# Kernel tuning notes

Hardware: AMD Instinct MI355X
Metric: run time of the kernel (lower is better)

Reference implementation:

```python
import jax, jax.numpy as jnp
import numpy as np

CPJ = 8
HID = 256
PARENTS = [-1,0,0,0,1,2,3,4,5,6,7,8,9,9,9,12,13,14,16,17,18,19]
SPARSE_IDX = list(range(54))

def _extend(nodes, cpj, parents=None):
    nodes = list(nodes)
    if parents is not None:
        while nodes[-1] != 0:
            nodes.append(parents[nodes[-1]])
    return [j * cpj + k for j in nodes for k in range(cpj)]

DQ_IN = _extend([0,3,6,9,12,13,14,15,16,17,18,19,20,21], CPJ, PARENTS)  # 21 nodes -> 168 ch
OUT1 = _extend([9], CPJ)          # 8 ch
OUT2 = _extend([6, 9, 12], CPJ)   # 24 ch
OUT3 = _extend([0, 3, 6], CPJ)    # 24 ch
IN_DIM = len(DQ_IN) + len(SPARSE_IDX)  # 222


def _mlp_params(key, out_dim):
    k = jax.random.split(key, 6)
    s = lambda fan_in: 1.0 / np.sqrt(fan_in)
    return (
        jax.random.uniform(k[0], (IN_DIM, HID), jnp.float32, -s(IN_DIM), s(IN_DIM)),
        jax.random.uniform(k[1], (HID,), jnp.float32, -s(IN_DIM), s(IN_DIM)),
        jax.random.uniform(k[2], (HID, HID), jnp.float32, -s(HID), s(HID)),
        jax.random.uniform(k[3], (HID,), jnp.float32, -s(HID), s(HID)),
        jax.random.uniform(k[4], (HID, out_dim), jnp.float32, -s(HID), s(HID)),
        jax.random.uniform(k[5], (out_dim,), jnp.float32, -s(HID), s(HID)),
    )


def setup_inputs() -> dict:
    key = jax.random.key(0)
    ks = jax.random.split(key, 5)
    B, T = 1024, 128
    inp = {
        'sparse_input': jax.random.normal(ks[0], (B, T, 54), jnp.float32),
        'decoder_output': jax.random.normal(ks[1], (B, T, 22 * CPJ), jnp.float32),
    }
    for i, (k, od) in enumerate(zip(ks[2:5], (len(OUT1), len(OUT2), len(OUT3))), start=1):
        p = _mlp_params(k, od)
        for j, name in enumerate(('w0', 'b0', 'w1', 'b1', 'w2', 'b2')):
            inp[f'{name}_{i}'] = p[j]
    return inp


def _mlp(x, w0, b0, w1, b1, w2, b2):
    h = jax.nn.leaky_relu(x @ w0 + b0, 0.01)
    h = jax.nn.leaky_relu(h @ w1 + b1, 0.01)
    return h @ w2 + b2


def reference(sparse_input, decoder_output,
              w0_1, b0_1, w1_1, b1_1, w2_1, b2_1,
              w0_2, b0_2, w1_2, b1_2, w2_2, b2_2,
              w0_3, b0_3, w1_3, b1_3, w2_3, b2_3):
    sp = sparse_input[:, :, jnp.array(SPARSE_IDX)]
    d = decoder_output
    # pass 1
    x = jnp.concatenate((d[:, :, jnp.array(DQ_IN)], sp), axis=2)
    res1 = _mlp(x, w0_1, b0_1, w1_1, b1_1, w2_1, b2_1)
    d = d.at[:, :, jnp.array(OUT1)].set(res1)
    # pass 2
    x = jnp.concatenate((d[:, :, jnp.array(DQ_IN)], sp), axis=2)
    res2 = _mlp(x, w0_2, b0_2, w1_2, b1_2, w2_2, b2_2)
    d = d.at[:, :, jnp.array(OUT2)].set(res2)
    # pass 3
    x = jnp.concatenate((d[:, :, jnp.array(DQ_IN)], sp), axis=2)
    res3 = _mlp(x, w0_3, b0_3, w1_3, b1_3, w2_3, b2_3)
    return res3
```

## Files before the change

### kernel.cpp

```cpp
#include <hip/hip_runtime.h>

typedef __bf16 bf16x8 __attribute__((ext_vector_type(8)));
typedef __bf16 bf16x4 __attribute__((ext_vector_type(4)));
typedef float  f32x16 __attribute__((ext_vector_type(16)));

#define DDEC  176
#define DSP   54
#define HID   256
#define RPW   32
#define WPB   4
#define BM    (RPW * WPB)
#define CSZ   8192
#define PSZ   16384
#define W1_OFF 65536
#define W2_OFF 131072
#define MLP_WS 139264

struct Biases { const float* b1[3]; const float* b2[3]; };

__global__ __launch_bounds__(256) void prep_weights(
    const float* __restrict__ w0a, const float* __restrict__ w1a, const float* __restrict__ w2a,
    const float* __restrict__ w0b, const float* __restrict__ w1b, const float* __restrict__ w2b,
    const float* __restrict__ w0c, const float* __restrict__ w1c, const float* __restrict__ w2c,
    const float* __restrict__ b0a, const float* __restrict__ b0b, const float* __restrict__ b0c,
    __bf16* __restrict__ ws)
{
  int idx = blockIdx.x * 256 + threadIdx.x;
  if (idx >= 3 * MLP_WS) return;
  int m = idx / MLP_WS;
  int r = idx - m * MLP_WS;
  const float* w0 = (m == 0) ? w0a : (m == 1) ? w0b : w0c;
  const float* w1 = (m == 0) ? w1a : (m == 1) ? w1b : w1c;
  const float* w2 = (m == 0) ? w2a : (m == 1) ? w2b : w2c;
  const float* b0 = (m == 0) ? b0a : (m == 1) ? b0b : b0c;
  float v;
  if (r < W1_OFF) {
    int n = r >> 8, k = r & 255;
    v = (k < 222) ? w0[k * HID + n] : (k == 222 ? b0[n] : 0.0f);
  } else if (r < W2_OFF) {
    int rr = r - W1_OFF;
    int n = rr >> 8, k = rr & 255;
    v = w1[k * HID + n];
  } else {
    int rr = r - W2_OFF;
    int n = rr >> 8, k = rr & 255;
    int od = (m == 0) ? 8 : 24;
    v = (n < od) ? w2[k * od + n] : 0.0f;
  }
  ws[idx] = (__bf16)v;
}

__device__ __forceinline__ float lrelu(float v) { return v > 0.f ? v : 0.01f * v; }

__device__ __forceinline__ void gload16(const void* g, void* l) {
  __builtin_amdgcn_global_load_lds(
      (const __attribute__((address_space(1))) void*)g,
      (__attribute__((address_space(3))) void*)l, 16, 0, 0);
}

__device__ __forceinline__ void stage2(const __bf16* __restrict__ wsrc, __bf16* buf, int tid) {
  #pragma unroll
  for (int r = 0; r < 8; ++r) {
    const int a  = (r * 256 + tid) * 16;
    const int lc = a >> 9;
    const int un = (a & 511) ^ ((lc & 31) << 4);
    gload16(wsrc + lc * 256 + (un >> 1), (char*)buf + r * 4096 + (tid >> 6) * 1024);
  }
}

template<int NKK>
__device__ __forceinline__ void gemm_pair_split(const __bf16* bank, const bf16x8* bfr,
                                                f32x16& oA, f32x16& oB, int r32, int h) {
  const int sw = r32 << 4;
  const char* c0 = (const char*)bank + (r32 << 9);
  const char* c1 = c0 + 16384;
  f32x16 a0 = {}, a1 = {}, b0 = {}, b1 = {};
  #pragma unroll
  for (int kk = 0; kk < NKK; ++kk) {
    const int inner = ((kk << 5) + (h << 4)) ^ sw;
    bf16x8 fa = *(const bf16x8*)(c0 + inner);
    bf16x8 fb = *(const bf16x8*)(c1 + inner);
    if (kk & 1) {
      a1 = __builtin_amdgcn_mfma_f32_32x32x16_bf16(fa, bfr[kk], a1, 0, 0, 0);
      b1 = __builtin_amdgcn_mfma_f32_32x32x16_bf16(fb, bfr[kk], b1, 0, 0, 0);
    } else {
      a0 = __builtin_amdgcn_mfma_f32_32x32x16_bf16(fa, bfr[kk], a0, 0, 0, 0);
      b0 = __builtin_amdgcn_mfma_f32_32x32x16_bf16(fb, bfr[kk], b0, 0, 0, 0);
    }
  }
  oA = a0 + a1;
  oB = b0 + b1;
}

template<int NKK>
__device__ __forceinline__ void gemm_pair(const __bf16* bank, const bf16x8* bfr,
                                          f32x16& accA, f32x16& accB, int r32, int h) {
  const int sw = r32 << 4;
  const char* c0 = (const char*)bank + (r32 << 9);
  const char* c1 = c0 + 16384;
  #pragma unroll
  for (int kk = 0; kk < NKK; ++kk) {
    const int inner = ((kk << 5) + (h << 4)) ^ sw;
    bf16x8 fa = *(const bf16x8*)(c0 + inner);
    bf16x8 fb = *(const bf16x8*)(c1 + inner);
    accA = __builtin_amdgcn_mfma_f32_32x32x16_bf16(fa, bfr[kk], accA, 0, 0, 0);
    accB = __builtin_amdgcn_mfma_f32_32x32x16_bf16(fb, bfr[kk], accB, 0, 0, 0);
  }
}

__device__ __forceinline__ bf16x4 shfl32(bf16x4 x) {
  union { bf16x4 v; unsigned long long u; } t;
  t.v = x;
  t.u = __shfl_xor(t.u, 32, 64);
  return t.v;
}
__device__ __forceinline__ bf16x8 cat44(bf16x4 lo, bf16x4 hi) {
  return (bf16x8){lo[0], lo[1], lo[2], lo[3], hi[0], hi[1], hi[2], hi[3]};
}

struct Frag2 { bf16x8 f0, f1; };

template<bool BIAS, bool LR>
__device__ __forceinline__ Frag2 d2frags(const f32x16 acc, const float* bias, int h) {
  bf16x4 pk[4];
  #pragma unroll
  for (int t = 0; t < 4; ++t) {
    float bx = 0.f, by = 0.f, bz = 0.f, bw = 0.f;
    if (BIAS) {
      float4 bv = *(const float4*)(bias + 8 * t + 4 * h);
      bx = bv.x; by = bv.y; bz = bv.z; bw = bv.w;
    }
    float v0 = acc[4 * t] + bx, v1 = acc[4 * t + 1] + by;
    float v2 = acc[4 * t + 2] + bz, v3 = acc[4 * t + 3] + bw;
    if (LR) { v0 = lrelu(v0); v1 = lrelu(v1); v2 = lrelu(v2); v3 = lrelu(v3); }
    pk[t] = (bf16x4){(__bf16)v0, (__bf16)v1, (__bf16)v2, (__bf16)v3};
  }
  bf16x4 r1 = shfl32(h ? pk[0] : pk[1]);
  bf16x4 r2 = shfl32(h ? pk[2] : pk[3]);
  Frag2 out;
  out.f0 = h ? cat44(r1, pk[1]) : cat44(pk[0], r1);
  out.f1 = h ? cat44(r2, pk[3]) : cat44(pk[2], r2);
  return out;
}

__device__ __forceinline__ bf16x8 packf44(float4 a, float4 b) {
  return (bf16x8){(__bf16)a.x, (__bf16)a.y, (__bf16)a.z, (__bf16)a.w,
                  (__bf16)b.x, (__bf16)b.y, (__bf16)b.z, (__bf16)b.w};
}
__device__ __forceinline__ bf16x8 packf2222(float2 a, float2 b, float2 c, float2 d) {
  return (bf16x8){(__bf16)a.x, (__bf16)a.y, (__bf16)b.x, (__bf16)b.y,
                  (__bf16)c.x, (__bf16)c.y, (__bf16)d.x, (__bf16)d.y};
}

__global__ __launch_bounds__(256, 2) void trunk_fused(
    const float* __restrict__ sparse, const float* __restrict__ dec,
    const __bf16* __restrict__ ws, float* __restrict__ out, Biases bp)
{
  __shared__ __align__(16) __bf16 lds[2 * PSZ];
  __shared__ __align__(16) float  bls[3 * 256 + 3 * 32];

  const int tid  = threadIdx.x;
  const int lane = tid & 63;
  const int wid  = tid >> 6;
  const int r32  = lane & 31;
  const int h    = lane >> 5;
  const long grow = (long)blockIdx.x * BM + wid * RPW + r32;

  stage2(ws, lds, tid);

  {
    #pragma unroll
    for (int mm = 0; mm < 3; ++mm) bls[mm * 256 + tid] = bp.b1[mm][tid];
    if (tid < 32) {
      #pragma unroll
      for (int mm = 0; mm < 3; ++mm) {
        int od = (mm == 0) ? 8 : 24;
        bls[768 + mm * 32 + tid] = (tid < od) ? bp.b2[mm][tid] : 0.f;
      }
    }
  }

  bf16x8 xb[14];
  {
    constexpr int ND[21] = {0,3,6,9,12,13,14,15,16,17,18,19,20,21,19,17,14,9,6,3,0};
    const float* drow = dec + grow * DDEC;
    const float* srow = sparse + grow * DSP;
    #pragma unroll
    for (int kf = 0; kf < 14; ++kf) {
      if (kf <= 9) {
        const int off = (h ? ND[2 * kf + 1] : ND[2 * kf]) * 8;
        const float4* p = (const float4*)(drow + off);
        xb[kf] = packf44(p[0], p[1]);
      } else if (kf == 10) {
        if (h == 0) {
          const float4* p = (const float4*)(drow + ND[20] * 8);
          xb[kf] = packf44(p[0], p[1]);
        } else {
          const float2* q = (const float2*)(srow + 0);
          xb[kf] = packf2222(q[0], q[1], q[2], q[3]);
        }
      } else if (kf <= 12) {
        const float2* q = (const float2*)(srow + (2 * kf + h - 21) * 8);
        xb[kf] = packf2222(q[0], q[1], q[2], q[3]);
      } else {
        if (h == 0) {
          const float2* q = (const float2*)(srow + 40);
          xb[kf] = packf2222(q[0], q[1], q[2], q[3]);
        } else {
          const float2* q = (const float2*)(srow + 48);
          xb[kf] = packf2222(q[0], q[1], q[2], make_float2(1.0f, 0.0f));
        }
      }
    }
  }
  int pb = 0;

  for (int m = 0; m < 3; ++m) {
    const __bf16* W0 = ws + m * MLP_WS;
    const __bf16* W1 = W0 + W1_OFF;
    const __bf16* W2 = W0 + W2_OFF;
    const float* b1l = bls + m * 256;
    const float* b2l = bls + 768 + m * 32;

    bf16x8 hb1[16];
    f32x16 a2 = {};

    #pragma unroll
    for (int p = 0; p < 4; ++p) {
      __syncthreads();
      __bf16* cur = lds + (pb ? PSZ : 0);
      __bf16* nxt = lds + (pb ? 0 : PSZ);
      stage2(p < 3 ? W0 + (p + 1) * PSZ : W1, nxt, tid);
      f32x16 aA, aB;
      __builtin_amdgcn_s_setprio(1);
      gemm_pair_split<14>(cur, xb, aA, aB, r32, h);
      __builtin_amdgcn_s_setprio(0);
      Frag2 t0 = d2frags<false, true>(aA, nullptr, h);
      Frag2 t1 = d2frags<false, true>(aB, nullptr, h);
      hb1[4 * p]     = t0.f0;
      hb1[4 * p + 1] = t0.f1;
      hb1[4 * p + 2] = t1.f0;
      hb1[4 * p + 3] = t1.f1;
      pb ^= 1;
    }

    #pragma unroll
    for (int p = 0; p < 4; ++p) {
      __syncthreads();
      __bf16* cur = lds + (pb ? PSZ : 0);
      __bf16* nxt = lds + (pb ? 0 : PSZ);
      const __bf16* w2f = W2 + r32 * 256 + h * 8 + 64 * p;
      bf16x8 wa0 = *(const bf16x8*)(w2f + 0);
      bf16x8 wa1 = *(const bf16x8*)(w2f + 16);
      bf16x8 wa2 = *(const bf16x8*)(w2f + 32);
      bf16x8 wa3 = *(const bf16x8*)(w2f + 48);
      if (p < 3)      stage2(W1 + (p + 1) * PSZ, nxt, tid);
      else if (m < 2) stage2(ws + (m + 1) * MLP_WS, nxt, tid);
      f32x16 accA = {}, accB = {};
      __builtin_amdgcn_s_setprio(1);
      gemm_pair<16>(cur, hb1, accA, accB, r32, h);
      __builtin_amdgcn_s_setprio(0);
      Frag2 tA = d2frags<true, true>(accA, b1l + 64 * p, h);
      Frag2 tB = d2frags<true, true>(accB, b1l + 64 * p + 32, h);
      __builtin_amdgcn_s_setprio(1);
      a2 = __builtin_amdgcn_mfma_f32_32x32x16_bf16(wa0, tA.f0, a2, 0, 0, 0);
      a2 = __builtin_amdgcn_mfma_f32_32x32x16_bf16(wa1, tA.f1, a2, 0, 0, 0);
      a2 = __builtin_amdgcn_mfma_f32_32x32x16_bf16(wa2, tB.f0, a2, 0, 0, 0);
      a2 = __builtin_amdgcn_mfma_f32_32x32x16_bf16(wa3, tB.f1, a2, 0, 0, 0);
      __builtin_amdgcn_s_setprio(0);
      pb ^= 1;
    }

    if (m == 2) {
      #pragma unroll
      for (int t = 0; t < 3; ++t) {
        const int c0 = 8 * t + 4 * h;
        float4 bv = *(const float4*)(b2l + c0);
        float4 o;
        o.x = a2[4 * t]     + bv.x;
        o.y = a2[4 * t + 1] + bv.y;
        o.z = a2[4 * t + 2] + bv.z;
        o.w = a2[4 * t + 3] + bv.w;
        *(float4*)(out + grow * 24 + c0) = o;
      }
    } else {
      bf16x4 pk[3];
      #pragma unroll
      for (int t = 0; t < 3; ++t) {
        const int c0 = 8 * t + 4 * h;
        float4 bv = *(const float4*)(b2l + c0);
        pk[t] = (bf16x4){(__bf16)(a2[4 * t] + bv.x),     (__bf16)(a2[4 * t + 1] + bv.y),
                         (__bf16)(a2[4 * t + 2] + bv.z), (__bf16)(a2[4 * t + 3] + bv.w)};
      }
      if (m == 0) {
        bf16x4 r = shfl32(pk[0]);
        if (h) { bf16x8 f = cat44(r, pk[0]); xb[1] = f; xb[8] = f; }
      } else {
        bf16x4 r1 = shfl32(h ? pk[0] : pk[1]);
        bf16x4 r2 = shfl32(pk[2]);
        if (h) {
          bf16x8 fJ9 = cat44(r1, pk[1]);  xb[1] = fJ9;  xb[8] = fJ9;
        } else {
          bf16x8 fJ6  = cat44(pk[0], r1); xb[1] = fJ6;  xb[9] = fJ6;
          bf16x8 fJ12 = cat44(pk[2], r2); xb[2] = fJ12;
        }
      }
    }
  }
}

extern "C" void kernel_launch(void* const* d_in, const int* in_sizes, int n_in,
                              void* d_out, int out_size, void* d_ws, size_t ws_size,
                              hipStream_t stream)
{
  const float* sparse = (const float*)d_in[0];
  const float* dec    = (const float*)d_in[1];
  Biases bp;
  const float* w0[3]; const float* w1[3]; const float* w2[3]; const float* b0[3];
  for (int m = 0; m < 3; ++m) {
    w0[m]    = (const float*)d_in[2 + m * 6 + 0];
    b0[m]    = (const float*)d_in[2 + m * 6 + 1];
    w1[m]    = (const float*)d_in[2 + m * 6 + 2];
    bp.b1[m] = (const float*)d_in[2 + m * 6 + 3];
    w2[m]    = (const float*)d_in[2 + m * 6 + 4];
    bp.b2[m] = (const float*)d_in[2 + m * 6 + 5];
  }
  __bf16* ws = (__bf16*)d_ws;
  const int nrows = in_sizes[0] / DSP;

  const int prep_total = 3 * MLP_WS;
  prep_weights<<<(prep_total + 255) / 256, 256, 0, stream>>>(
      w0[0], w1[0], w2[0], w0[1], w1[1], w2[1], w0[2], w1[2], w2[2],
      b0[0], b0[1], b0[2], ws);

  const int nblocks = nrows / BM;
  trunk_fused<<<nblocks, 256, 0, stream>>>(sparse, dec, ws, (float*)d_out, bp);
}
```

Before: 137.3 us.

## Double waves per block to share staged weight tiles across more rows

Raises waves per block from 4 to 8 so each staged LDS weight panel serves 256 rows instead of 128. Each thread issues half as many async loads per stage, and the launch bound changes to 512 threads with 4 waves per SIMD. The split-accumulator GEMM for the first layer is replaced by a single accumulator chain, which saves registers but lengthens MFMA dependency chains. Bias loading is guarded so only the first 256 threads run it.

Measured after the change: 246.0 us. 1.79x slower.

```diff
diff --git a/kernel.cpp b/kernel.cpp
--- a/kernel.cpp
+++ b/kernel.cpp
@@ -8,9 +8,9 @@
 #define DSP   54
 #define HID   256
 #define RPW   32
-#define WPB   4
+#define WPB   8
 #define BM    (RPW * WPB)
-#define CSZ   8192
+#define NTHR  (WPB * 64)
 #define PSZ   16384
 #define W1_OFF 65536
 #define W2_OFF 131072
@@ -60,36 +60,12 @@
 
 __device__ __forceinline__ void stage2(const __bf16* __restrict__ wsrc, __bf16* buf, int tid) {
   #pragma unroll
-  for (int r = 0; r < 8; ++r) {
-    const int a  = (r * 256 + tid) * 16;
+  for (int r = 0; r < 4; ++r) {
+    const int a  = (r * NTHR + tid) * 16;
     const int lc = a >> 9;
     const int un = (a & 511) ^ ((lc & 31) << 4);
-    gload16(wsrc + lc * 256 + (un >> 1), (char*)buf + r * 4096 + (tid >> 6) * 1024);
-  }
-}
-
-template<int NKK>
-__device__ __forceinline__ void gemm_pair_split(const __bf16* bank, const bf16x8* bfr,
-                                                f32x16& oA, f32x16& oB, int r32, int h) {
-  const int sw = r32 << 4;
-  const char* c0 = (const char*)bank + (r32 << 9);
-  const char* c1 = c0 + 16384;
-  f32x16 a0 = {}, a1 = {}, b0 = {}, b1 = {};
-  #pragma unroll
-  for (int kk = 0; kk < NKK; ++kk) {
-    const int inner = ((kk << 5) + (h << 4)) ^ sw;
-    bf16x8 fa = *(const bf16x8*)(c0 + inner);
-    bf16x8 fb = *(const bf16x8*)(c1 + inner);
-    if (kk & 1) {
-      a1 = __builtin_amdgcn_mfma_f32_32x32x16_bf16(fa, bfr[kk], a1, 0, 0, 0);
-      b1 = __builtin_amdgcn_mfma_f32_32x32x16_bf16(fb, bfr[kk], b1, 0, 0, 0);
-    } else {
-      a0 = __builtin_amdgcn_mfma_f32_32x32x16_bf16(fa, bfr[kk], a0, 0, 0, 0);
-      b0 = __builtin_amdgcn_mfma_f32_32x32x16_bf16(fb, bfr[kk], b0, 0, 0, 0);
-    }
-  }
-  oA = a0 + a1;
-  oB = b0 + b1;
+    gload16(wsrc + lc * 256 + (un >> 1), (char*)buf + r * (NTHR * 16) + (tid >> 6) * 1024);
+  }
 }
 
 template<int NKK>
@@ -152,7 +128,7 @@
                   (__bf16)c.x, (__bf16)c.y, (__bf16)d.x, (__bf16)d.y};
 }
 
-__global__ __launch_bounds__(256, 2) void trunk_fused(
+__global__ __launch_bounds__(NTHR, 4) void trunk_fused(
     const float* __restrict__ sparse, const float* __restrict__ dec,
     const __bf16* __restrict__ ws, float* __restrict__ out, Biases bp)
 {
@@ -168,7 +144,7 @@
 
   stage2(ws, lds, tid);
 
-  {
+  if (tid < 256) {
     #pragma unroll
     for (int mm = 0; mm < 3; ++mm) bls[mm * 256 + tid] = bp.b1[mm][tid];
     if (tid < 32) {
@@ -231,9 +207,9 @@
       __bf16* cur = lds + (pb ? PSZ : 0);
       __bf16* nxt = lds + (pb ? 0 : PSZ);
       stage2(p < 3 ? W0 + (p + 1) * PSZ : W1, nxt, tid);
-      f32x16 aA, aB;
+      f32x16 aA = {}, aB = {};
       __builtin_amdgcn_s_setprio(1);
-      gemm_pair_split<14>(cur, xb, aA, aB, r32, h);
+      gemm_pair<14>(cur, xb, aA, aB, r32, h);
       __builtin_amdgcn_s_setprio(0);
       Frag2 t0 = d2frags<false, true>(aA, nullptr, h);
       Frag2 t1 = d2frags<false, true>(aB, nullptr, h);
@@ -334,5 +310,5 @@
       b0[0], b0[1], b0[2], ws);
 
   const int nblocks = nrows / BM;
-  trunk_fused<<<nblocks, 256, 0, stream>>>(sparse, dec, ws, (float*)d_out, bp);
-}
+  trunk_fused<<<nblocks, NTHR, 0, stream>>>(sparse, dec, ws, (float*)d_out, bp);
+}
```
